# Kernel optimization log

Measured on AMD Instinct MI355X. Metric: run time of the kernel, lower is better.

The kernel has to match this reference:

```python
import jax, jax.numpy as jnp
import numpy as np

N, D, E, T, R, KMEM, DE = 50000, 128, 800000, 400000, 1, 32, 16
EPS = 1e-5
BETA_MAX = 5.0
GRAD_CLIP = 1.0
STATE_CLIP = 10.0
STEP = 0.1
DAMP = 0.9999  # update_damping=1.0 clamped to 1-1e-4 as in __init__


def segment_logsumexp(s, idx, n):
    # numerically-stable per-segment logsumexp; empty segments contribute 0
    m = jax.ops.segment_max(s, idx, num_segments=n)
    ms = jnp.where(jnp.isfinite(m), m, 0.0)
    z = jax.ops.segment_sum(jnp.exp(s - ms[idx]), idx, num_segments=n)
    return jnp.where(z > 0, jnp.log(jnp.maximum(z, 1e-30)) + ms, 0.0)


def setup_inputs() -> dict:
    key = jax.random.key(0)
    ks = jax.random.split(key, 24)
    inv1 = jnp.log(jnp.expm1(jnp.float32(1.0)))  # _inv_softplus(1.0)
    xav = 0.5 * np.sqrt(2.0 / (2 * D))  # xavier_uniform gain=0.5 ~ std
    inp = {
        'X': jax.random.normal(ks[0], (N, D), jnp.float32),
        'edge_attr': jax.random.normal(ks[1], (E, DE), jnp.float32),
        'ln_gamma': jnp.ones((D,), jnp.float32),
        'ln_beta': jnp.zeros((D,), jnp.float32),
        'W_Q2': jax.random.normal(ks[2], (D, D), jnp.float32) * xav,
        'W_K2': jax.random.normal(ks[3], (D, D), jnp.float32) * xav,
        'W_Q3': jax.random.normal(ks[4], (D, R * D), jnp.float32) * xav,
        'W_K3': jax.random.normal(ks[5], (D, R * D), jnp.float32) * xav,
        'T_tau': jax.random.normal(ks[6], (2, R, D), jnp.float32) * 0.02,
        'W_Qm': jax.random.normal(ks[7], (D, D), jnp.float32) * xav,
        'W_Km': jax.random.normal(ks[8], (D, D), jnp.float32) * xav,
        'B_mem': jax.random.normal(ks[9], (KMEM, D), jnp.float32) / np.sqrt(D),
        'We1': jax.random.normal(ks[10], (DE, D), jnp.float32) / np.sqrt(DE),
        'be1': jnp.zeros((D,), jnp.float32),
        'We2': jax.random.normal(ks[11], (D, 1), jnp.float32) / np.sqrt(D),
        'be2': jnp.zeros((1,), jnp.float32),
        'lambda_2': inv1, 'lambda_3': inv1, 'lambda_m': inv1,
        'beta_2': inv1, 'beta_3': inv1, 'beta_m': inv1,
        'c_2': jax.random.randint(ks[12], (E,), 0, N),
        'u_2': jax.random.randint(ks[13], (E,), 0, N),
        'c_3': jax.random.randint(ks[14], (T,), 0, N),
        'u_3': jax.random.randint(ks[15], (T,), 0, N),
        'v_3': jax.random.randint(ks[16], (T,), 0, N),
        't_tau': jax.random.randint(ks[17], (T,), 0, 2),
    }
    return inp


def reference(X, edge_attr, ln_gamma, ln_beta, W_Q2, W_K2, W_Q3, W_K3, T_tau,
              W_Qm, W_Km, B_mem, We1, be1, We2, be2,
              lambda_2, lambda_3, lambda_m, beta_2, beta_3, beta_m,
              c_2, u_2, c_3, u_3, v_3, t_tau):
    sqrt_d = jnp.sqrt(jnp.float32(D))

    def energy(Xv):
        mu = jnp.mean(Xv, axis=-1, keepdims=True)
        var = jnp.var(Xv, axis=-1, keepdims=True)
        G = (Xv - mu) * jax.lax.rsqrt(var + EPS) * ln_gamma + ln_beta
        # pairwise (order-2) energy over edge list
        b2 = jnp.minimum(jax.nn.softplus(beta_2), BETA_MAX)
        Q2, K2 = G @ W_Q2, G @ W_K2
        a2 = (jax.nn.gelu(edge_attr @ We1 + be1) @ We2 + be2)[:, 0]  # edge_mlp bias
        s2 = b2 * (jnp.sum(Q2[c_2] * K2[u_2], axis=-1) / sqrt_d) + a2  # [E]
        E2 = -(jax.nn.softplus(lambda_2) / b2) * jnp.sum(segment_logsumexp(s2, c_2, N))
        # triplet (order-3) energy with per-type tensor T_tau
        b3 = jnp.minimum(jax.nn.softplus(beta_3), BETA_MAX)
        Q3 = (G @ W_Q3).reshape(-1, R, D)
        K3 = (G @ W_K3).reshape(-1, R, D)
        s3 = b3 * jnp.einsum('erd,erd,erd,erd->e', Q3[c_3], K3[u_3], K3[v_3],
                             T_tau[t_tau]) / jnp.float32(D)  # [T]
        E3 = -(jax.nn.softplus(lambda_3) / b3) * jnp.sum(segment_logsumexp(s3, c_3, N))
        # memory-bank energy
        bm = jnp.minimum(jax.nn.softplus(beta_m), BETA_MAX)
        sm = bm * ((G @ W_Qm) @ (B_mem @ W_Km).T) / sqrt_d  # [N,K]
        Em = -(jax.nn.softplus(lambda_m) / bm) * jnp.sum(jax.nn.logsumexp(sm, axis=1))
        return E2 + E3 + Em

    Eval, gX = jax.value_and_grad(energy)(X)
    gn = jnp.maximum(jnp.linalg.norm(gX, axis=-1, keepdims=True), 1e-6)
    gX = gX * jnp.minimum(GRAD_CLIP / gn, 1.0)
    X_next = X - STEP * DAMP * gX
    sn = jnp.maximum(jnp.linalg.norm(X_next, axis=-1, keepdims=True), 1e-6)
    X_next = X_next * jnp.minimum(STATE_CLIP / sn, 1.0)
    return (X_next, Eval)
```

## Files before the change

### kernel.cpp

```cpp
#include <hip/hip_runtime.h>

#define NN 50000
#define DD 128
#define EE 800000
#define TT 400000
#define KM 32
#define UU 320
#define ROWB 12500
#define MB 782
#define EDGE_BLKS 3125
#define SCAN_TILE 2048
#define SCAN_NB ((NN + SCAN_TILE - 1) / SCAN_TILE)

static constexpr float INV_SQRT_D = 0.08838834764831845f;
static constexpr float INV_D = 1.f / 128.f;

typedef __attribute__((ext_vector_type(8))) short bf16x8;
typedef __attribute__((ext_vector_type(4))) float f32x4;
typedef unsigned short ushort_t;

__device__ __forceinline__ float softplus_f(float x) {
  return (x > 20.f) ? x : log1pf(__expf(x));
}

__device__ __forceinline__ float gelu_fast(float x) {
  float p = fmaf(0.044715f * x * x, x, x);
  float e = __expf(-1.5957691216057308f * p);
  return x * __builtin_amdgcn_rcpf(1.f + e);
}

__device__ __forceinline__ float wredsum(float v) {
#pragma unroll
  for (int m = 32; m; m >>= 1) v += __shfl_xor(v, m, 64);
// ... 8 lines not shown

__device__ __forceinline__ float blo(unsigned w) { return __uint_as_float(w << 16); }
__device__ __forceinline__ float bhi(unsigned w) { return __uint_as_float(w & 0xffff0000u); }
__device__ __forceinline__ unsigned pack_bf16(float a, float b) {
  unsigned ua = __float_as_uint(a); ua += 0x7fff + ((ua >> 16) & 1);
  unsigned ub = __float_as_uint(b); ub += 0x7fff + ((ub >> 16) & 1);
  return (ua >> 16) | (ub & 0xffff0000u);
}
__device__ __forceinline__ ushort_t bf16_1(float x) {
  unsigned u = __float_as_uint(x); u += 0x7fff + ((u >> 16) & 1);
  return (ushort_t)(u >> 16);
}
__device__ __forceinline__ void unp8(uint4 w, float* f) {
  f[0] = blo(w.x); f[1] = bhi(w.x); f[2] = blo(w.y); f[3] = bhi(w.y);
  f[4] = blo(w.z); f[5] = bhi(w.z); f[6] = blo(w.w); f[7] = bhi(w.w);
}
__device__ __forceinline__ uint4 pk8(const float* f) {
  uint4 r;
  r.x = pack_bf16(f[0], f[1]); r.y = pack_bf16(f[2], f[3]);
  r.z = pack_bf16(f[4], f[5]); r.w = pack_bf16(f[6], f[7]);
  return r;
}

__global__ void params_k(const float* l2, const float* l3, const float* lm,
                         const float* b2, const float* b3, const float* bm,
                         float* __restrict__ P) {
  if (threadIdx.x != 0) return;
  float B2 = fminf(softplus_f(b2[0]), 5.f);
  float B3 = fminf(softplus_f(b3[0]), 5.f);
  float Bm = fminf(softplus_f(bm[0]), 5.f);
  float S2 = softplus_f(l2[0]);
  float S3 = softplus_f(l3[0]);
  float Sm = softplus_f(lm[0]);
  P[0] = B2; P[1] = B3; P[2] = Bm;
  P[3] = -S2 * INV_SQRT_D; P[4] = -S3 * INV_D; P[5] = -Sm * INV_SQRT_D;
  P[6] = -S2 / B2; P[7] = -S3 / B3; P[8] = -Sm / Bm;
}

__global__ __launch_bounds__(256) void ln_fwd(const float* __restrict__ X,
                                              const float* __restrict__ gamma,
                                              const float* __restrict__ beta,
                                              unsigned* __restrict__ Gb,
                                              float* __restrict__ meanv,
                                              float* __restrict__ rstdv) {
  int row = blockIdx.x * 4 + (threadIdx.x >> 6);
  if (row >= NN) return;
  int l = threadIdx.x & 63;
  float2 x2 = *(const float2*)(X + row * DD + 2 * l);
  float mu = wredsum(x2.x + x2.y) * (1.f / DD);
  float d0 = x2.x - mu, d1 = x2.y - mu;
  float var = wredsum(d0 * d0 + d1 * d1) * (1.f / DD);
  float rstd = rsqrtf(var + 1e-5f);
  float2 g2 = *(const float2*)(gamma + 2 * l);
  float2 b2 = *(const float2*)(beta + 2 * l);
  float o0 = d0 * rstd * g2.x + b2.x;
  float o1 = d1 * rstd * g2.y + b2.y;
  Gb[(size_t)row * 64 + l] = pack_bf16(o0, o1);
  if (l == 0) { meanv[row] = mu; rstdv[row] = rstd; }
}

__global__ __launch_bounds__(256) void w_conv(const float* W0, const float* W1, const float* W2,
                                              const float* W3, const float* W4,
                                              ushort_t* __restrict__ Wt,
                                              ushort_t* __restrict__ Wc) {
  int idx = blockIdx.x * 256 + threadIdx.x;
  if (idx >= 640 * 128) return;
  const float* Ws[5] = {W0, W1, W2, W3, W4};
  int n = idx >> 7, k = idx & 127;
  Wt[idx] = bf16_1(Ws[n >> 7][(size_t)k * 128 + (n & 127)]);
  int k2 = idx >> 7, n2 = idx & 127;
  Wc[(size_t)n2 * 640 + k2] = bf16_1(Ws[k2 >> 7][(size_t)n2 * 128 + (k2 & 127)]);
}

__device__ void mfma_fwd_body(int bxr, int by, const ushort_t* __restrict__ Gb,
                              const ushort_t* __restrict__ Wt,
                              ushort_t* __restrict__ QK, int M) {
  __shared__ ushort_t sB[64][136];
  int tid = threadIdx.x;
  int nb = by * 64;
  for (int idx = tid; idx < 64 * 16; idx += 256) {
    int r = idx >> 4, c8 = idx & 15;
    *(bf16x8*)&sB[r][c8 * 8] = *(const bf16x8*)(Wt + (size_t)(nb + r) * 128 + c8 * 8);
  }
  __syncthreads();
  int w = tid >> 6, l = tid & 63, quad = l >> 4, j = l & 15;
  int row0 = bxr * 64 + w * 16;
  int arow = row0 + j; if (arow >= M) arow = M - 1;
  const bf16x8* ap = (const bf16x8*)(Gb + (size_t)arow * 128);
  f32x4 acc[4];
#pragma unroll
  for (int nt = 0; nt < 4; nt++) acc[nt] = (f32x4){0.f, 0.f, 0.f, 0.f};
#pragma unroll
  for (int kc = 0; kc < 4; kc++) {
    bf16x8 a = ap[kc * 4 + quad];
// ... 60 lines not shown
    float s0 = 0.f, s1 = 0.f, s2 = 0.f, s3 = 0.f;
#pragma unroll
    for (int nt = 0; nt < 8; nt++) {
      float bias = bb[nt];
      f32x4 cin = (f32x4){bias, bias, bias, bias};
      f32x4 acc = __builtin_amdgcn_mfma_f32_16x16x32_bf16(af.v, bf[nt].v, cin, 0, 0, 0);
      float w2v = ww[nt];
      s0 = fmaf(gelu_fast(acc[0]), w2v, s0);
      s1 = fmaf(gelu_fast(acc[1]), w2v, s1);
      s2 = fmaf(gelu_fast(acc[2]), w2v, s2);
      s3 = fmaf(gelu_fast(acc[3]), w2v, s3);
    }
    s0 = redsum16(s0); s1 = redsum16(s1); s2 = redsum16(s2); s3 = redsum16(s3);
    if (m == 0) {
      int eb = e0 + q * 4;
      a2[eb + 0] = s0 + be2v;
      a2[eb + 1] = s1 + be2v;
      a2[eb + 2] = s2 + be2v;
      a2[eb + 3] = s3 + be2v;
    }
  }
}

__global__ __launch_bounds__(256) void fwd_k(const ushort_t* __restrict__ Gb,
                                             const ushort_t* __restrict__ Wt,
                                             ushort_t* __restrict__ QK,
                                             const float* __restrict__ EA,
                                             const float* __restrict__ We1,
                                             const float* __restrict__ be1,
                                             const float* __restrict__ We2,
                                             const float* __restrict__ be2,
                                             float* __restrict__ a2) {
  int bx = blockIdx.x;
  if (bx < MB * 10) {
    mfma_fwd_body(bx / 10, bx % 10, Gb, Wt, QK, NN);
  } else {
    edge_mlp_body(bx - MB * 10, EA, We1, be1, We2, be2, a2);
  }
}

__global__ __launch_bounds__(256) void mfma_bwd(const ushort_t* __restrict__ dAll,
                                                const ushort_t* __restrict__ Wc,
                                                unsigned* __restrict__ dG, int M) {
  __shared__ ushort_t sB[64][40];
  int tid = threadIdx.x;
  int nb = blockIdx.y * 64;
  int w = tid >> 6, l = tid & 63, quad = l >> 4, j = l & 15;
  int row0 = blockIdx.x * 64 + w * 16;
  int arow = row0 + j; if (arow >= M) arow = M - 1;
  const ushort_t* arp = dAll + (size_t)arow * 640;
  f32x4 acc[4];
#pragma unroll
  for (int nt = 0; nt < 4; nt++) acc[nt] = (f32x4){0.f, 0.f, 0.f, 0.f};
  int sr = tid >> 2, sc = tid & 3;
  for (int kc = 0; kc < 20; kc++) {
    __syncthreads();
    *(bf16x8*)&sB[sr][sc * 8] = *(const bf16x8*)(Wc + (size_t)(nb + sr) * 640 + kc * 32 + sc * 8);
    __syncthreads();
    bf16x8 a = *(const bf16x8*)(arp + kc * 32 + quad * 8);
#pragma unroll
    for (int nt = 0; nt < 4; nt++) {
      bf16x8 b = *(const bf16x8*)&sB[nt * 16 + j][quad * 8];
      acc[nt] = __builtin_amdgcn_mfma_f32_16x16x32_bf16(a, b, acc[nt], 0, 0, 0);
    }
  }
#pragma unroll
  for (int nt = 0; nt < 4; nt++)
#pragma unroll
    for (int r = 0; r < 4; r++) {
      int row = row0 + quad * 4 + r;
      if (row < M) ((ushort_t*)dG)[(size_t)row * 128 + nb + nt * 16 + j] = bf16_1(acc[nt][r]);
    }
}

__global__ __launch_bounds__(256, 1) void gemm_km(const float* __restrict__ A,
                                                  const float* __restrict__ W,
                                                  float* __restrict__ C, int M) {
  __shared__ float As[32][132];
  __shared__ float Wst[128][136];
  const int tid = threadIdx.x;
  for (int idx = tid; idx < 128 * 128; idx += 256) {
    int k = idx >> 7, jj = idx & 127;
    Wst[k][jj] = W[k * 128 + jj];
  }
  for (int idx = tid; idx < 32 * 128; idx += 256) {
    int r = idx >> 7, d = idx & 127;
    As[r][d] = A[r * 128 + d];
  }
  __syncthreads();
  int r = tid >> 3, c0 = (tid & 7) * 16;
  float acc[16];
#pragma unroll
  for (int q = 0; q < 16; q++) acc[q] = 0.f;
  for (int k = 0; k < 128; k++) {
    float av = As[r][k];
#pragma unroll
    for (int q = 0; q < 16; q++) acc[q] = fmaf(av, Wst[k][c0 + q], acc[q]);
  }
#pragma unroll
  for (int q = 0; q < 16; q++) C[r * 128 + c0 + q] = acc[q];
}

__global__ __launch_bounds__(256) void hist2(const int* __restrict__ a,
                                             const int* __restrict__ b,
                                             int* __restrict__ ca,
                                             int* __restrict__ cb,
                                             int* __restrict__ pos_a,
                                             int* __restrict__ pos_b, int n) {
  int base = blockIdx.x * 2048 + threadIdx.x;
  if (base + 1792 < n) {
    int av[8], bv[8], pa[8], pb[8];
#pragma unroll
    for (int k = 0; k < 8; k++) { int e = base + k * 256; av[k] = a[e]; bv[k] = b[e]; }
#pragma unroll
    for (int k = 0; k < 8; k++) pa[k] = atomicAdd(&ca[av[k]], 1);
#pragma unroll
    for (int k = 0; k < 8; k++) pb[k] = atomicAdd(&cb[bv[k]], 1);
#pragma unroll
    for (int k = 0; k < 8; k++) pos_a[base + k * 256] = pa[k];
#pragma unroll
    for (int k = 0; k < 8; k++) pos_b[base + k * 256] = pb[k];
  } else {
#pragma unroll
    for (int k = 0; k < 8; k++) {
      int e = base + k * 256;
      if (e < n) {
        pos_a[e] = atomicAdd(&ca[a[e]], 1);
        pos_b[e] = atomicAdd(&cb[b[e]], 1);
      }
    }
  }
}

__global__ __launch_bounds__(256) void hist_t3(const int* __restrict__ c,
                                               const int* __restrict__ u,
                                               const int* __restrict__ v,
                                               int* __restrict__ cc,
                                               int* __restrict__ cuv,
                                               int* __restrict__ pos_c,
                                               int* __restrict__ pos_u,
                                               int* __restrict__ pos_v, int n) {
  int base = blockIdx.x * 2048 + threadIdx.x;
  if (base + 1792 < n) {
    int cv[8], uv[8], vv[8], pc[8], pu[8], pv[8];
#pragma unroll
    for (int k = 0; k < 8; k++) { int t = base + k * 256; cv[k] = c[t]; uv[k] = u[t]; vv[k] = v[t]; }
#pragma unroll
    for (int k = 0; k < 8; k++) pc[k] = atomicAdd(&cc[cv[k]], 1);
#pragma unroll
    for (int k = 0; k < 8; k++) pu[k] = atomicAdd(&cuv[uv[k]], 1);
#pragma unroll
    for (int k = 0; k < 8; k++) pv[k] = atomicAdd(&cuv[vv[k]], 1);
#pragma unroll
    for (int k = 0; k < 8; k++) pos_c[base + k * 256] = pc[k];
#pragma unroll
    for (int k = 0; k < 8; k++) pos_u[base + k * 256] = pu[k];
#pragma unroll
    for (int k = 0; k < 8; k++) pos_v[base + k * 256] = pv[k];
  } else {
#pragma unroll
    for (int k = 0; k < 8; k++) {
      int t = base + k * 256;
      if (t < n) {
        pos_c[t] = atomicAdd(&cc[c[t]], 1);
        pos_u[t] = atomicAdd(&cuv[u[t]], 1);
        pos_v[t] = atomicAdd(&cuv[v[t]], 1);
      }
    }
  }
}

__global__ __launch_bounds__(256) void scan_p1(const int* __restrict__ cnt,
                                               int* __restrict__ part) {
  int arr = blockIdx.y, b = blockIdx.x;
  const int* c = cnt + (size_t)arr * NN;
  int gi = b * SCAN_TILE + threadIdx.x * 8;
  int s = 0;
#pragma unroll
  for (int t = 0; t < 8; t++) s += (gi + t < NN) ? c[gi + t] : 0;
#pragma unroll
  for (int m = 32; m; m >>= 1) s += __shfl_xor(s, m, 64);
  __shared__ int wt[4];
  int lane = threadIdx.x & 63, wid = threadIdx.x >> 6;
  if (lane == 0) wt[wid] = s;
  __syncthreads();
  if (threadIdx.x == 0) part[arr * SCAN_NB + b] = wt[0] + wt[1] + wt[2] + wt[3];
}

__global__ __launch_bounds__(256) void scan_p2(int* __restrict__ part) {
  int w = threadIdx.x >> 6, l = threadIdx.x & 63;
  int v = (l < SCAN_NB) ? part[w * SCAN_NB + l] : 0;
  int x = v;
#pragma unroll
  for (int d = 1; d < 64; d <<= 1) {
// ... 18 lines not shown
#pragma unroll
  for (int t = 0; t < 8; t++) tsum += vals[t];
  int lane = tid & 63, wid = tid >> 6;
  int x = tsum;
#pragma unroll
  for (int d = 1; d < 64; d <<= 1) {
    int y = __shfl_up(x, d, 64);
    if (lane >= d) x += y;
  }
  __shared__ int wt[4];
  if (lane == 63) wt[wid] = x;
  __syncthreads();
  int wadd = 0;
  for (int w = 0; w < wid; w++) wadd += wt[w];
  int running = part[arr * SCAN_NB + b] + wadd + x - tsum;
#pragma unroll
  for (int t = 0; t < 8; t++) {
    if (gi + t < NN) rp[gi + t] = running;
    running += vals[t];
  }
  if (b == SCAN_NB - 1 && tid == 255) rp[NN] = running;
}

__global__ __launch_bounds__(256) void scat2(const int* __restrict__ c2,
                                             const int* __restrict__ u2,
                                             const float* __restrict__ a2,
                                             const int* __restrict__ posc,
                                             const int* __restrict__ posu,
                                             const int* __restrict__ rpc,
                                             const int* __restrict__ rpu,
                                             uint2* __restrict__ payc,
                                             uint2* __restrict__ payu, int n) {
  int base = blockIdx.x * 2048 + threadIdx.x;
  if (base + 1792 < n) {
    int c[8], u[8]; float a[8]; int pc[8], pu[8];
#pragma unroll
    for (int k = 0; k < 8; k++) {
      int e = base + k * 256;
      c[k] = c2[e]; u[k] = u2[e]; a[k] = a2[e]; pc[k] = posc[e]; pu[k] = posu[e];
    }
    int p[8], q[8];
#pragma unroll
    for (int k = 0; k < 8; k++) { p[k] = rpc[c[k]] + pc[k]; q[k] = rpu[u[k]] + pu[k]; }
#pragma unroll
    for (int k = 0; k < 8; k++) {
      uint2 t; t.x = (unsigned)u[k]; t.y = __float_as_uint(a[k]);
      payc[p[k]] = t;
    }
#pragma unroll
    for (int k = 0; k < 8; k++) {
      uint2 t; t.x = (unsigned)p[k]; t.y = (unsigned)c[k];
      payu[q[k]] = t;
    }
  } else {
#pragma unroll
    for (int k = 0; k < 8; k++) {
      int e = base + k * 256;
      if (e < n) {
        int cc = c2[e], uu = u2[e];
        int pp = rpc[cc] + posc[e];
        int qq = rpu[uu] + posu[e];
        uint2 t; t.x = (unsigned)uu; t.y = __float_as_uint(a2[e]);
        payc[pp] = t;
        uint2 t2; t2.x = (unsigned)pp; t2.y = (unsigned)cc;
        payu[qq] = t2;
      }
    }
  }
}

__global__ __launch_bounds__(256) void scat_t3(const int* __restrict__ c3,
                                               const int* __restrict__ u3,
                                               const int* __restrict__ v3,
                                               const int* __restrict__ ttau,
                                               const int* __restrict__ posc,
                                               const int* __restrict__ posu,
                                               const int* __restrict__ posv,
                                               const int* __restrict__ rpc,
                                               const int* __restrict__ rpuv,
                                               uint2* __restrict__ payc,
                                               uint2* __restrict__ payuv, int n) {
  int base = blockIdx.x * 2048 + threadIdx.x;
  if (base + 1792 < n) {
    int c[8], u[8], v[8], ta[8], p[8], q1[8], q2[8];
#pragma unroll
    for (int k = 0; k < 8; k++) {
      int t = base + k * 256;
      c[k] = c3[t]; u[k] = u3[t]; v[k] = v3[t]; ta[k] = ttau[t] & 1;
    }
#pragma unroll
    for (int k = 0; k < 8; k++) {
      int t = base + k * 256;
      p[k] = rpc[c[k]] + posc[t];
      q1[k] = rpuv[u[k]] + posu[t];
      q2[k] = rpuv[v[k]] + posv[t];
    }
#pragma unroll
    for (int k = 0; k < 8; k++) {
      uint2 a; a.x = ((unsigned)u[k] << 16) | (unsigned)v[k]; a.y = (unsigned)ta[k];
      payc[p[k]] = a;
    }
#pragma unroll
    for (int k = 0; k < 8; k++) {
      unsigned sp = ((unsigned)p[k] << 1) | (unsigned)ta[k];
      uint2 b1; b1.x = ((unsigned)v[k] << 16) | (unsigned)c[k]; b1.y = sp;
      payuv[q1[k]] = b1;
      uint2 b2; b2.x = ((unsigned)u[k] << 16) | (unsigned)c[k]; b2.y = sp;
      payuv[q2[k]] = b2;
    }
  } else {
#pragma unroll
    for (int k = 0; k < 8; k++) {
      int t = base + k * 256;
      if (t < n) {
        int c = c3[t], u = u3[t], v = v3[t], ta = ttau[t] & 1;
        int p = rpc[c] + posc[t];
        int q1 = rpuv[u] + posu[t];
        int q2 = rpuv[v] + posv[t];
        unsigned sp = ((unsigned)p << 1) | (unsigned)ta;
        uint2 a; a.x = ((unsigned)u << 16) | (unsigned)v; a.y = (unsigned)ta;
        payc[p] = a;
        uint2 b1; b1.x = ((unsigned)v << 16) | (unsigned)c; b1.y = sp;
        payuv[q1] = b1;
        uint2 b2; b2.x = ((unsigned)u << 16) | (unsigned)c; b2.y = sp;
        payuv[q2] = b2;
      }
    }
  }
}

__device__ void e2_body(int bx, const unsigned* __restrict__ QK,
                        const float* __restrict__ P,
                        const uint2* __restrict__ pay,
                        const int* __restrict__ rp,
                        float* __restrict__ s2c,
                        float* __restrict__ L2,
                        unsigned* __restrict__ dAll) {
  int row = bx * 4 + (threadIdx.x >> 6);
  int l = threadIdx.x & 63, g = l >> 4, j = l & 15;
  float b2s = P[0] * INV_SQRT_D, cw2 = P[3];
  float q[8];
  unp8(*(const uint4*)(QK + (size_t)row * UU + j * 4), q);
  int s = rp[row], e = rp[row + 1];
  float m = -3.0e38f, z = 0.f;
  float acc[8] = {0.f, 0.f, 0.f, 0.f, 0.f, 0.f, 0.f, 0.f};
  int i0 = s + g;
  uint4 kA1 = {0,0,0,0}, kA2 = {0,0,0,0}, kB1 = {0,0,0,0}, kB2 = {0,0,0,0};
  float aA1 = 0.f, aA2 = 0.f, aB1 = 0.f, aB2 = 0.f;
  if (i0 < e)      { uint2 w = pay[i0];      aA1 = __uint_as_float(w.y); kA1 = *(const uint4*)(QK + (size_t)w.x * UU + 64 + j * 4); }
  if (i0 + 4 < e)  { uint2 w = pay[i0 + 4];  aA2 = __uint_as_float(w.y); kA2 = *(const uint4*)(QK + (size_t)w.x * UU + 64 + j * 4); }
// ... 204 lines not shown
    v += __shfl_xor(v, 16, 64);
    v += __shfl_xor(v, 32, 64);
    acc[t] = v;
  }
  if (g == 0) *(uint4*)(dAll + (size_t)row * UU + 256 + j * 4) = pk8(acc);
}

__global__ __launch_bounds__(256) void phase2_k(const unsigned* __restrict__ QK,
                                                const float* __restrict__ Tt,
                                                const float* __restrict__ Km,
                                                const float* __restrict__ P,
                                                const uint2* __restrict__ payc2,
                                                const int* __restrict__ rp_c2,
                                                const uint2* __restrict__ payc3,
                                                const int* __restrict__ rp_c3,
                                                float* __restrict__ s2c,
                                                float* __restrict__ L2,
                                                float* __restrict__ s3c,
                                                float* __restrict__ L3,
                                                float* __restrict__ Lm,
                                                unsigned* __restrict__ dAll) {
  __shared__ float smem[32 * 144];
  int bx = blockIdx.x;
  int tid = threadIdx.x;
  if (bx < ROWB) {
    e2_body(bx, QK, P, payc2, rp_c2, s2c, L2, dAll);
  } else if (bx < 2 * ROWB) {
    {
      int ta = tid >> 7, d = tid & 127;
      smem[ta * 144 + (d >> 3) * 9 + (d & 7)] = Tt[tid];
    }
    __syncthreads();
    t3_body(bx - ROWB, QK, P, payc3, rp_c3, s3c, L3, dAll, smem);
  } else {
    for (int i = tid; i < KM * DD; i += 256) {
      int k = i >> 7, d = i & 127;
      smem[k * 144 + (d >> 3) * 9 + (d & 7)] = Km[i];
    }
    __syncthreads();
    em_body(bx - 2 * ROWB, QK, P, dAll, Lm, smem);
  }
}

__device__ void dk2_body(int bx, const unsigned* __restrict__ QK,
                         const float* __restrict__ s2c,
                         const float* __restrict__ L2,
                         const float* __restrict__ P,
                         const uint2* __restrict__ pay,
                         const int* __restrict__ rp,
                         unsigned* __restrict__ dAll) {
  int row = bx * 4 + (threadIdx.x >> 6);
  int l = threadIdx.x & 63, g = l >> 4, j = l & 15;
  float cw2 = P[3];
  int s = rp[row], e = rp[row + 1];
  float acc[8] = {0.f, 0.f, 0.f, 0.f, 0.f, 0.f, 0.f, 0.f};
  int i0 = s + g;
  uint4 qA1 = {0,0,0,0}, qA2 = {0,0,0,0}, qB1 = {0,0,0,0}, qB2 = {0,0,0,0};
  float scA1 = 0.f, lcA1 = 0.f, scA2 = 0.f, lcA2 = 0.f;
  float scB1 = 0.f, lcB1 = 0.f, scB2 = 0.f, lcB2 = 0.f;
  if (i0 < e)      { uint2 w = pay[i0];      scA1 = s2c[w.x]; lcA1 = L2[w.y]; qA1 = *(const uint4*)(QK + (size_t)w.y * UU + 0 + j * 4); }
  if (i0 + 4 < e)  { uint2 w = pay[i0 + 4];  scA2 = s2c[w.x]; lcA2 = L2[w.y]; qA2 = *(const uint4*)(QK + (size_t)w.y * UU + 0 + j * 4); }
  if (i0 + 8 < e)  { uint2 w = pay[i0 + 8];  scB1 = s2c[w.x]; lcB1 = L2[w.y]; qB1 = *(const uint4*)(QK + (size_t)w.y * UU + 0 + j * 4); }
  if (i0 + 12 < e) { uint2 w = pay[i0 + 12]; scB2 = s2c[w.x]; lcB2 = L2[w.y]; qB2 = *(const uint4*)(QK + (size_t)w.y * UU + 0 + j * 4); }
// ... 79 lines not shown
  for (int t = 0; t < 8; t++) {
    float v = acc[t];
    v += __shfl_xor(v, 16, 64);
    v += __shfl_xor(v, 32, 64);
    acc[t] = v;
  }
  if (g == 0) *(uint4*)(dAll + (size_t)row * UU + 192 + j * 4) = pk8(acc);
}

__global__ __launch_bounds__(256) void phase3_k(const unsigned* __restrict__ QK,
                                                const float* __restrict__ Tt,
                                                const float* __restrict__ P,
                                                const float* __restrict__ s2c,
                                                const float* __restrict__ L2,
                                                const uint2* __restrict__ payu2,
                                                const int* __restrict__ rp_u2,
                                                const float* __restrict__ s3c,
                                                const float* __restrict__ L3,
                                                const uint2* __restrict__ payuv,
                                                const int* __restrict__ rp_uv,
                                                unsigned* __restrict__ dAll) {
  __shared__ float smem[2 * 144];
  int bx = blockIdx.x;
  int tid = threadIdx.x;
  if (bx < ROWB) {
    dk2_body(bx, QK, s2c, L2, P, payu2, rp_u2, dAll);
  } else {
    {
      int ta = tid >> 7, d = tid & 127;
      smem[ta * 144 + (d >> 3) * 9 + (d & 7)] = Tt[tid];
    }
    __syncthreads();
    dk3_body(bx - ROWB, QK, s3c, L3, P, payuv, rp_uv, dAll, smem);
  }
}

__global__ __launch_bounds__(256) void ln_bwd(const float* __restrict__ X,
                                              const unsigned* __restrict__ dG,
                                              const float* __restrict__ gamma,
                                              const float* __restrict__ meanv,
                                              const float* __restrict__ rstdv,
                                              float* __restrict__ out) {
  int row = blockIdx.x * 4 + (threadIdx.x >> 6);
  if (row >= NN) return;
  int l = threadIdx.x & 63;
  float mu = meanv[row], rstd = rstdv[row];
  float2 x2 = *(const float2*)(X + row * DD + 2 * l);
  unsigned gw = dG[(size_t)row * 64 + l];
  float2 ga = *(const float2*)(gamma + 2 * l);
  float xh0 = (x2.x - mu) * rstd, xh1 = (x2.y - mu) * rstd;
  float dh0 = blo(gw) * ga.x, dh1 = bhi(gw) * ga.y;
  float sa = wredsum(dh0 + dh1) * (1.f / DD);
  float sb = wredsum(dh0 * xh0 + dh1 * xh1) * (1.f / DD);
  float dx0 = rstd * (dh0 - sa - xh0 * sb);
  float dx1 = rstd * (dh1 - sa - xh1 * sb);
  float gn = fmaxf(sqrtf(wredsum(dx0 * dx0 + dx1 * dx1)), 1e-6f);
  float sc = fminf(1.f / gn, 1.f);
  dx0 *= sc; dx1 *= sc;
  float xn0 = x2.x - 0.1f * 0.9999f * dx0;
  float xn1 = x2.y - 0.1f * 0.9999f * dx1;
  float sn = fmaxf(sqrtf(wredsum(xn0 * xn0 + xn1 * xn1)), 1e-6f);
  float sc2 = fminf(10.f / sn, 1.f);
  float2 o; o.x = xn0 * sc2; o.y = xn1 * sc2;
  *(float2*)(out + row * DD + 2 * l) = o;
}

__global__ __launch_bounds__(256) void eval_write(const float* __restrict__ L2,
                                                  const float* __restrict__ L3,
                                                  const float* __restrict__ Lm,
                                                  const float* __restrict__ P,
                                                  float* __restrict__ out) {
  int i = blockIdx.x * 256 + threadIdx.x;
  float a2 = 0.f, a3 = 0.f, am = 0.f;
  if (i < NN) { a2 = L2[i]; a3 = L3[i]; am = Lm[i]; }
  a2 = wredsum(a2); a3 = wredsum(a3); am = wredsum(am);
  __shared__ float r2[4], r3[4], rm[4];
  int wv = threadIdx.x >> 6, l = threadIdx.x & 63;
  if (l == 0) { r2[wv] = a2; r3[wv] = a3; rm[wv] = am; }
  __syncthreads();
  if (threadIdx.x == 0) {
    float S2 = r2[0] + r2[1] + r2[2] + r2[3];
    float S3 = r3[0] + r3[1] + r3[2] + r3[3];
    float Sm = rm[0] + rm[1] + rm[2] + rm[3];
    atomicAdd(out, P[6] * S2 + P[7] * S3 + P[8] * Sm);
  }
}

extern "C" void kernel_launch(void* const* d_in, const int* in_sizes, int n_in,
                              void* d_out, int out_size, void* d_ws, size_t ws_size,
                              hipStream_t stream) {
  (void)in_sizes; (void)n_in; (void)out_size;
  const float* X = (const float*)d_in[0];
  const float* EA = (const float*)d_in[1];
  const float* ln_g = (const float*)d_in[2];
  const float* ln_b = (const float*)d_in[3];
  const float* W_Q2 = (const float*)d_in[4];
  const float* W_K2 = (const float*)d_in[5];
  const float* W_Q3 = (const float*)d_in[6];
  const float* W_K3 = (const float*)d_in[7];
  const float* T_tau = (const float*)d_in[8];
  const float* W_Qm = (const float*)d_in[9];
  const float* W_Km = (const float*)d_in[10];
  const float* B_mem = (const float*)d_in[11];
  const float* We1 = (const float*)d_in[12];
  const float* be1 = (const float*)d_in[13];
  const float* We2 = (const float*)d_in[14];
  const float* be2 = (const float*)d_in[15];
  const float* l2s = (const float*)d_in[16];
// ... 27 lines not shown
  float* meanv = alloc(NN);
  float* rstdv = alloc(NN);
  float* L2 = alloc(NN);
  float* L3 = alloc(NN);
  float* Lm = alloc(NN);
  float* Pparams = alloc(16);
  int* cnt = (int*)alloc(4 * (size_t)NN);
  int* rowptr = (int*)alloc(4 * (size_t)(NN + 1));
  int* spart = (int*)alloc(4 * SCAN_NB);
  int* pos_c2 = (int*)alloc(EE);
  int* pos_u2 = (int*)alloc(EE);
  int* pos_c3 = (int*)alloc(TT);
  int* pos_u3 = (int*)alloc(TT);
  int* pos_v3 = (int*)alloc(TT);
  uint2* payc2 = (uint2*)alloc(2 * (size_t)EE);
  uint2* payu2 = (uint2*)alloc(2 * (size_t)EE);
  uint2* payc3 = (uint2*)alloc(2 * (size_t)TT);
  uint2* payuv = (uint2*)alloc(4 * (size_t)TT);
  if (off * sizeof(float) > ws_size) return;

  int* cnt_c2 = cnt, *cnt_u2 = cnt + NN, *cnt_c3 = cnt + 2 * NN, *cnt_uv = cnt + 3 * NN;
  int* rp_c2 = rowptr, *rp_u2 = rowptr + (NN + 1), *rp_c3 = rowptr + 2 * (NN + 1), *rp_uv = rowptr + 3 * (NN + 1);

  hipMemsetAsync(cnt, 0, 4ull * NN * sizeof(int), stream);
  hipMemsetAsync(out + ND, 0, sizeof(float), stream);

  params_k<<<1, 64, 0, stream>>>(l2s, l3s, lms, b2s, b3s, bms, Pparams);

  int rowB = ROWB;

  ln_fwd<<<rowB, 256, 0, stream>>>(X, ln_g, ln_b, Gb, meanv, rstdv);
  w_conv<<<320, 256, 0, stream>>>(W_Q2, W_K2, W_Q3, W_K3, W_Qm, Wt5, Wcat);
  gemm_km<<<1, 256, 0, stream>>>(B_mem, W_Km, Km, KM);
  fwd_k<<<MB * 10 + EDGE_BLKS, 256, 0, stream>>>((const ushort_t*)Gb, Wt5, (ushort_t*)QKall,
                                                 EA, We1, be1, We2, be2, a2);

  hist2<<<(EE + 2047) / 2048, 256, 0, stream>>>(c2, u2, cnt_c2, cnt_u2, pos_c2, pos_u2, EE);
  hist_t3<<<(TT + 2047) / 2048, 256, 0, stream>>>(c3, u3, v3, cnt_c3, cnt_uv,
                                                  pos_c3, pos_u3, pos_v3, TT);
  scan_p1<<<dim3(SCAN_NB, 4), 256, 0, stream>>>(cnt, spart);
  scan_p2<<<1, 256, 0, stream>>>(spart);
  scan_p3<<<dim3(SCAN_NB, 4), 256, 0, stream>>>(cnt, spart, rowptr);
  scat2<<<(EE + 2047) / 2048, 256, 0, stream>>>(c2, u2, a2, pos_c2, pos_u2,
                                                rp_c2, rp_u2, payc2, payu2, EE);
  scat_t3<<<(TT + 2047) / 2048, 256, 0, stream>>>(c3, u3, v3, ttau,
                                                  pos_c3, pos_u3, pos_v3,
                                                  rp_c3, rp_uv, payc3, payuv, TT);

  phase2_k<<<3 * ROWB, 256, 0, stream>>>(QKall, T_tau, Km, Pparams,
                                         payc2, rp_c2, payc3, rp_c3,
                                         s2c, L2, s3c, L3, Lm, dAll);
  phase3_k<<<2 * ROWB, 256, 0, stream>>>(QKall, T_tau, Pparams,
                                         s2c, L2, payu2, rp_u2,
                                         s3c, L3, payuv, rp_uv, dAll);

  mfma_bwd<<<dim3(MB, 2), 256, 0, stream>>>((const ushort_t*)dAll, Wcat, dG, NN);

  ln_bwd<<<rowB, 256, 0, stream>>>(X, dG, ln_g, meanv, rstdv, out);
  eval_write<<<(NN + 255) / 256, 256, 0, stream>>>(L2, L3, Lm, Pparams, out + ND);
}
```

Measured before the change: 766.9 us.

## Merge small kernels into fused multi-role launches and interleave phase block roles

Measured after the change: 765.2 us. No clear change (-0.2%).

```diff
diff --git a/kernel.cpp b/kernel.cpp
--- a/kernel.cpp
+++ b/kernel.cpp
@@ -9,6 +9,10 @@
 #define ROWB 12500
 #define MB 782
 #define EDGE_BLKS 3125
+#define HB2 391
+#define HBT 196
+#define WCB 320
+#define ZCB 196
 #define SCAN_TILE 2048
 #define SCAN_NB ((NN + SCAN_TILE - 1) / SCAN_TILE)
 
@@ -63,28 +67,13 @@
   return r;
 }
 
-__global__ void params_k(const float* l2, const float* l3, const float* lm,
-                         const float* b2, const float* b3, const float* bm,
-                         float* __restrict__ P) {
-  if (threadIdx.x != 0) return;
-  float B2 = fminf(softplus_f(b2[0]), 5.f);
-  float B3 = fminf(softplus_f(b3[0]), 5.f);
-  float Bm = fminf(softplus_f(bm[0]), 5.f);
-  float S2 = softplus_f(l2[0]);
-  float S3 = softplus_f(l3[0]);
-  float Sm = softplus_f(lm[0]);
-  P[0] = B2; P[1] = B3; P[2] = Bm;
-  P[3] = -S2 * INV_SQRT_D; P[4] = -S3 * INV_D; P[5] = -Sm * INV_SQRT_D;
-  P[6] = -S2 / B2; P[7] = -S3 / B3; P[8] = -Sm / Bm;
-}
-
-__global__ __launch_bounds__(256) void ln_fwd(const float* __restrict__ X,
-                                              const float* __restrict__ gamma,
-                                              const float* __restrict__ beta,
-                                              unsigned* __restrict__ Gb,
-                                              float* __restrict__ meanv,
-                                              float* __restrict__ rstdv) {
-  int row = blockIdx.x * 4 + (threadIdx.x >> 6);
+__device__ void ln_fwd_body(int bx, const float* __restrict__ X,
+                            const float* __restrict__ gamma,
+                            const float* __restrict__ beta,
+                            unsigned* __restrict__ Gb,
+                            float* __restrict__ meanv,
+                            float* __restrict__ rstdv) {
+  int row = bx * 4 + (threadIdx.x >> 6);
   if (row >= NN) return;
   int l = threadIdx.x & 63;
   float2 x2 = *(const float2*)(X + row * DD + 2 * l);
@@ -100,17 +89,87 @@
   if (l == 0) { meanv[row] = mu; rstdv[row] = rstd; }
 }
 
-__global__ __launch_bounds__(256) void w_conv(const float* W0, const float* W1, const float* W2,
-                                              const float* W3, const float* W4,
-                                              ushort_t* __restrict__ Wt,
-                                              ushort_t* __restrict__ Wc) {
-  int idx = blockIdx.x * 256 + threadIdx.x;
-  if (idx >= 640 * 128) return;
+__device__ void w_conv_body(int b, const float* W0, const float* W1, const float* W2,
+                            const float* W3, const float* W4,
+                            ushort_t* __restrict__ Wt,
+                            ushort_t* __restrict__ Wc) {
+  int idx = b * 256 + threadIdx.x;
   const float* Ws[5] = {W0, W1, W2, W3, W4};
   int n = idx >> 7, k = idx & 127;
   Wt[idx] = bf16_1(Ws[n >> 7][(size_t)k * 128 + (n & 127)]);
   int k2 = idx >> 7, n2 = idx & 127;
   Wc[(size_t)n2 * 640 + k2] = bf16_1(Ws[k2 >> 7][(size_t)n2 * 128 + (k2 & 127)]);
+}
+
+__device__ void gemm_km_lean(const float* __restrict__ A,
+                             const float* __restrict__ W,
+                             float* __restrict__ C) {
+  __shared__ float As[32][129];
+  int tid = threadIdx.x;
+  for (int idx = tid; idx < 32 * 128; idx += 256) As[idx >> 7][idx & 127] = A[idx];
+  __syncthreads();
+  int r = tid >> 3, c0 = (tid & 7) * 16;
+  float acc[16];
+#pragma unroll
+  for (int q = 0; q < 16; q++) acc[q] = 0.f;
+  for (int k = 0; k < 128; k++) {
+    float av = As[r][k];
+#pragma unroll
+    for (int q = 0; q < 16; q++) acc[q] = fmaf(av, W[k * 128 + c0 + q], acc[q]);
+  }
+#pragma unroll
+  for (int q = 0; q < 16; q++) C[r * 128 + c0 + q] = acc[q];
+}
+
+__global__ __launch_bounds__(256) void prep_k(const float* __restrict__ X,
+                                              const float* __restrict__ ln_g,
+                                              const float* __restrict__ ln_b,
+                                              unsigned* __restrict__ Gb,
+                                              float* __restrict__ meanv,
+                                              float* __restrict__ rstdv,
+                                              const float* W0, const float* W1,
+                                              const float* W2, const float* W3,
+                                              const float* W4,
+                                              ushort_t* __restrict__ Wt,
+                                              ushort_t* __restrict__ Wc,
+                                              const float* __restrict__ Bm,
+                                              const float* __restrict__ Wkm,
+                                              float* __restrict__ Km,
+                                              const float* l2, const float* l3,
+                                              const float* lm, const float* b2,
+                                              const float* b3, const float* bm,
+                                              float* __restrict__ P,
+                                              float* __restrict__ eout,
+                                              int* __restrict__ cnt) {
+  int bx = blockIdx.x, tid = threadIdx.x;
+  if (bx < ROWB) {
+    ln_fwd_body(bx, X, ln_g, ln_b, Gb, meanv, rstdv);
+  } else if (bx < ROWB + WCB) {
+    w_conv_body(bx - ROWB, W0, W1, W2, W3, W4, Wt, Wc);
+  } else if (bx == ROWB + WCB) {
+    gemm_km_lean(Bm, Wkm, Km);
+  } else if (bx == ROWB + WCB + 1) {
+    if (tid == 0) {
+      float B2 = fminf(softplus_f(b2[0]), 5.f);
+      float B3 = fminf(softplus_f(b3[0]), 5.f);
+      float Bm_ = fminf(softplus_f(bm[0]), 5.f);
+      float S2 = softplus_f(l2[0]);
+      float S3 = softplus_f(l3[0]);
+      float Sm = softplus_f(lm[0]);
+      P[0] = B2; P[1] = B3; P[2] = Bm_;
+      P[3] = -S2 * INV_SQRT_D; P[4] = -S3 * INV_D; P[5] = -Sm * INV_SQRT_D;
+      P[6] = -S2 / B2; P[7] = -S3 / B3; P[8] = -Sm / Bm_;
+    }
+    if (tid == 1) eout[0] = 0.f;
+  } else {
+    int i = (bx - (ROWB + WCB + 2)) * 1024 + tid * 4;
+    if (i + 3 < 4 * NN) {
+      *(int4*)&cnt[i] = (int4){0, 0, 0, 0};
+    } else {
+#pragma unroll
+      for (int t = 0; t < 4; t++) if (i + t < 4 * NN) cnt[i + t] = 0;
+    }
+  }
 }
 
 __device__ void mfma_fwd_body(int bxr, int by, const ushort_t* __restrict__ Gb,
@@ -217,6 +276,71 @@
   }
 }
 
+__device__ void hist2_body(int bx, const int* __restrict__ a,
+                           const int* __restrict__ b,
+                           int* __restrict__ ca, int* __restrict__ cb,
+                           int* __restrict__ pos_a, int* __restrict__ pos_b, int n) {
+  int base = bx * 2048 + threadIdx.x;
+  if (base + 1792 < n) {
+    int av[8], bv[8], pa[8], pb[8];
+#pragma unroll
+    for (int k = 0; k < 8; k++) { int e = base + k * 256; av[k] = a[e]; bv[k] = b[e]; }
+#pragma unroll
+    for (int k = 0; k < 8; k++) pa[k] = atomicAdd(&ca[av[k]], 1);
+#pragma unroll
+    for (int k = 0; k < 8; k++) pb[k] = atomicAdd(&cb[bv[k]], 1);
+#pragma unroll
+    for (int k = 0; k < 8; k++) pos_a[base + k * 256] = pa[k];
+#pragma unroll
+    for (int k = 0; k < 8; k++) pos_b[base + k * 256] = pb[k];
+  } else {
+#pragma unroll
+    for (int k = 0; k < 8; k++) {
+      int e = base + k * 256;
+      if (e < n) {
+        pos_a[e] = atomicAdd(&ca[a[e]], 1);
+        pos_b[e] = atomicAdd(&cb[b[e]], 1);
+      }
+    }
+  }
+}
+
+__device__ void hist_t3_body(int bx, const int* __restrict__ c,
+                             const int* __restrict__ u,
+                             const int* __restrict__ v,
+                             int* __restrict__ cc, int* __restrict__ cuv,
+                             int* __restrict__ pos_c, int* __restrict__ pos_u,
+                             int* __restrict__ pos_v, int n) {
+  int base = bx * 2048 + threadIdx.x;
+  if (base + 1792 < n) {
+    int cv[8], uv[8], vv[8], pc[8], pu[8], pv[8];
+#pragma unroll
+    for (int k = 0; k < 8; k++) { int t = base + k * 256; cv[k] = c[t]; uv[k] = u[t]; vv[k] = v[t]; }
+#pragma unroll
+    for (int k = 0; k < 8; k++) pc[k] = atomicAdd(&cc[cv[k]], 1);
+#pragma unroll
+    for (int k = 0; k < 8; k++) pu[k] = atomicAdd(&cuv[uv[k]], 1);
+#pragma unroll
+    for (int k = 0; k < 8; k++) pv[k] = atomicAdd(&cuv[vv[k]], 1);
+#pragma unroll
+    for (int k = 0; k < 8; k++) pos_c[base + k * 256] = pc[k];
+#pragma unroll
+    for (int k = 0; k < 8; k++) pos_u[base + k * 256] = pu[k];
+#pragma unroll
+    for (int k = 0; k < 8; k++) pos_v[base + k * 256] = pv[k];
+  } else {
+#pragma unroll
+    for (int k = 0; k < 8; k++) {
+      int t = base + k * 256;
+      if (t < n) {
+        pos_c[t] = atomicAdd(&cc[c[t]], 1);
+        pos_u[t] = atomicAdd(&cuv[u[t]], 1);
+        pos_v[t] = atomicAdd(&cuv[v[t]], 1);
+      }
+    }
+  }
+}
+
 __global__ __launch_bounds__(256) void fwd_k(const ushort_t* __restrict__ Gb,
                                              const ushort_t* __restrict__ Wt,
                                              ushort_t* __restrict__ QK,
@@ -225,12 +349,31 @@
                                              const float* __restrict__ be1,
                                              const float* __restrict__ We2,
                                              const float* __restrict__ be2,
-                                             float* __restrict__ a2) {
+                                             float* __restrict__ a2,
+                                             const int* __restrict__ c2,
+                                             const int* __restrict__ u2,
+                                             const int* __restrict__ c3,
+                                             const int* __restrict__ u3,
+                                             const int* __restrict__ v3,
+                                             int* __restrict__ cnt_c2,
+                                             int* __restrict__ cnt_u2,
+                                             int* __restrict__ cnt_c3,
+                                             int* __restrict__ cnt_uv,
+                                             int* __restrict__ pos_c2,
+                                             int* __restrict__ pos_u2,
+                                             int* __restrict__ pos_c3,
+                                             int* __restrict__ pos_u3,
+                                             int* __restrict__ pos_v3) {
   int bx = blockIdx.x;
-  if (bx < MB * 10) {
-    mfma_fwd_body(bx / 10, bx % 10, Gb, Wt, QK, NN);
+  if (bx < HB2) {
+    hist2_body(bx, c2, u2, cnt_c2, cnt_u2, pos_c2, pos_u2, EE);
+  } else if (bx < HB2 + HBT) {
+    hist_t3_body(bx - HB2, c3, u3, v3, cnt_c3, cnt_uv, pos_c3, pos_u3, pos_v3, TT);
+  } else if (bx < HB2 + HBT + MB * 10) {
+    int b = bx - HB2 - HBT;
+    mfma_fwd_body(b / 10, b % 10, Gb, Wt, QK, NN);
   } else {
-    edge_mlp_body(bx - MB * 10, EA, We1, be1, We2, be2, a2);
+    edge_mlp_body(bx - HB2 - HBT - MB * 10, EA, We1, be1, We2, be2, a2);
   }
 }
 
@@ -268,103 +411,6 @@
     }
 }
 
-__global__ __launch_bounds__(256, 1) void gemm_km(const float* __restrict__ A,
-                                                  const float* __restrict__ W,
-                                                  float* __restrict__ C, int M) {
-  __shared__ float As[32][132];
-  __shared__ float Wst[128][136];
-  const int tid = threadIdx.x;
-  for (int idx = tid; idx < 128 * 128; idx += 256) {
-    int k = idx >> 7, jj = idx & 127;
-    Wst[k][jj] = W[k * 128 + jj];
-  }
-  for (int idx = tid; idx < 32 * 128; idx += 256) {
-    int r = idx >> 7, d = idx & 127;
-    As[r][d] = A[r * 128 + d];
-  }
-  __syncthreads();
-  int r = tid >> 3, c0 = (tid & 7) * 16;
-  float acc[16];
-#pragma unroll
-  for (int q = 0; q < 16; q++) acc[q] = 0.f;
-  for (int k = 0; k < 128; k++) {
-    float av = As[r][k];
-#pragma unroll
-    for (int q = 0; q < 16; q++) acc[q] = fmaf(av, Wst[k][c0 + q], acc[q]);
-  }
-#pragma unroll
-  for (int q = 0; q < 16; q++) C[r * 128 + c0 + q] = acc[q];
-}
-
-__global__ __launch_bounds__(256) void hist2(const int* __restrict__ a,
-                                             const int* __restrict__ b,
-                                             int* __restrict__ ca,
-                                             int* __restrict__ cb,
-                                             int* __restrict__ pos_a,
-                                             int* __restrict__ pos_b, int n) {
-  int base = blockIdx.x * 2048 + threadIdx.x;
-  if (base + 1792 < n) {
-    int av[8], bv[8], pa[8], pb[8];
-#pragma unroll
-    for (int k = 0; k < 8; k++) { int e = base + k * 256; av[k] = a[e]; bv[k] = b[e]; }
-#pragma unroll
-    for (int k = 0; k < 8; k++) pa[k] = atomicAdd(&ca[av[k]], 1);
-#pragma unroll
-    for (int k = 0; k < 8; k++) pb[k] = atomicAdd(&cb[bv[k]], 1);
-#pragma unroll
-    for (int k = 0; k < 8; k++) pos_a[base + k * 256] = pa[k];
-#pragma unroll
-    for (int k = 0; k < 8; k++) pos_b[base + k * 256] = pb[k];
-  } else {
-#pragma unroll
-    for (int k = 0; k < 8; k++) {
-      int e = base + k * 256;
-      if (e < n) {
-        pos_a[e] = atomicAdd(&ca[a[e]], 1);
-        pos_b[e] = atomicAdd(&cb[b[e]], 1);
-      }
-    }
-  }
-}
-
-__global__ __launch_bounds__(256) void hist_t3(const int* __restrict__ c,
-                                               const int* __restrict__ u,
-                                               const int* __restrict__ v,
-                                               int* __restrict__ cc,
-                                               int* __restrict__ cuv,
-                                               int* __restrict__ pos_c,
-                                               int* __restrict__ pos_u,
-                                               int* __restrict__ pos_v, int n) {
-  int base = blockIdx.x * 2048 + threadIdx.x;
-  if (base + 1792 < n) {
-    int cv[8], uv[8], vv[8], pc[8], pu[8], pv[8];
-#pragma unroll
-    for (int k = 0; k < 8; k++) { int t = base + k * 256; cv[k] = c[t]; uv[k] = u[t]; vv[k] = v[t]; }
-#pragma unroll
-    for (int k = 0; k < 8; k++) pc[k] = atomicAdd(&cc[cv[k]], 1);
-#pragma unroll
-    for (int k = 0; k < 8; k++) pu[k] = atomicAdd(&cuv[uv[k]], 1);
-#pragma unroll
-    for (int k = 0; k < 8; k++) pv[k] = atomicAdd(&cuv[vv[k]], 1);
-#pragma unroll
-    for (int k = 0; k < 8; k++) pos_c[base + k * 256] = pc[k];
-#pragma unroll
-    for (int k = 0; k < 8; k++) pos_u[base + k * 256] = pu[k];
-#pragma unroll
-    for (int k = 0; k < 8; k++) pos_v[base + k * 256] = pv[k];
-  } else {
-#pragma unroll
-    for (int k = 0; k < 8; k++) {
-      int t = base + k * 256;
-      if (t < n) {
-        pos_c[t] = atomicAdd(&cc[c[t]], 1);
-        pos_u[t] = atomicAdd(&cuv[u[t]], 1);
-        pos_v[t] = atomicAdd(&cuv[v[t]], 1);
-      }
-    }
-  }
-}
-
 __global__ __launch_bounds__(256) void scan_p1(const int* __restrict__ cnt,
                                                int* __restrict__ part) {
   int arr = blockIdx.y, b = blockIdx.x;
@@ -429,16 +475,16 @@
   if (b == SCAN_NB - 1 && tid == 255) rp[NN] = running;
 }
 
-__global__ __launch_bounds__(256) void scat2(const int* __restrict__ c2,
-                                             const int* __restrict__ u2,
-                                             const float* __restrict__ a2,
-                                             const int* __restrict__ posc,
-                                             const int* __restrict__ posu,
-                                             const int* __restrict__ rpc,
-                                             const int* __restrict__ rpu,
-                                             uint2* __restrict__ payc,
-                                             uint2* __restrict__ payu, int n) {
-  int base = blockIdx.x * 2048 + threadIdx.x;
+__device__ void scat2_body(int bx, const int* __restrict__ c2,
+                           const int* __restrict__ u2,
+                           const float* __restrict__ a2,
+                           const int* __restrict__ posc,
+                           const int* __restrict__ posu,
+                           const int* __restrict__ rpc,
+                           const int* __restrict__ rpu,
+                           uint2* __restrict__ payc,
+                           uint2* __restrict__ payu, int n) {
+  int base = bx * 2048 + threadIdx.x;
   if (base + 1792 < n) {
     int c[8], u[8]; float a[8]; int pc[8], pu[8];
 #pragma unroll
@@ -476,18 +522,18 @@
   }
 }
 
-__global__ __launch_bounds__(256) void scat_t3(const int* __restrict__ c3,
-                                               const int* __restrict__ u3,
-                                               const int* __restrict__ v3,
-                                               const int* __restrict__ ttau,
-                                               const int* __restrict__ posc,
-                                               const int* __restrict__ posu,
-                                               const int* __restrict__ posv,
-                                               const int* __restrict__ rpc,
-                                               const int* __restrict__ rpuv,
-                                               uint2* __restrict__ payc,
-                                               uint2* __restrict__ payuv, int n) {
-  int base = blockIdx.x * 2048 + threadIdx.x;
+__device__ void scat_t3_body(int bx, const int* __restrict__ c3,
+                             const int* __restrict__ u3,
+                             const int* __restrict__ v3,
+                             const int* __restrict__ ttau,
+                             const int* __restrict__ posc,
+                             const int* __restrict__ posu,
+                             const int* __restrict__ posv,
+                             const int* __restrict__ rpc,
+                             const int* __restrict__ rpuv,
+                             uint2* __restrict__ payc,
+                             uint2* __restrict__ payuv, int n) {
+  int base = bx * 2048 + threadIdx.x;
   if (base + 1792 < n) {
     int c[8], u[8], v[8], ta[8], p[8], q1[8], q2[8];
 #pragma unroll
@@ -533,6 +579,35 @@
         payuv[q2] = b2;
       }
     }
+  }
+}
+
+__global__ __launch_bounds__(256) void scat_k(const int* __restrict__ c2,
+                                              const int* __restrict__ u2,
+                                              const float* __restrict__ a2,
+                                              const int* __restrict__ pos_c2,
+                                              const int* __restrict__ pos_u2,
+                                              const int* __restrict__ rp_c2,
+                                              const int* __restrict__ rp_u2,
+                                              uint2* __restrict__ payc2,
+                                              uint2* __restrict__ payu2,
+                                              const int* __restrict__ c3,
+                                              const int* __restrict__ u3,
+                                              const int* __restrict__ v3,
+                                              const int* __restrict__ ttau,
+                                              const int* __restrict__ pos_c3,
+                                              const int* __restrict__ pos_u3,
+                                              const int* __restrict__ pos_v3,
+                                              const int* __restrict__ rp_c3,
+                                              const int* __restrict__ rp_uv,
+                                              uint2* __restrict__ payc3,
+                                              uint2* __restrict__ payuv) {
+  int bx = blockIdx.x;
+  if (bx < HB2) {
+    scat2_body(bx, c2, u2, a2, pos_c2, pos_u2, rp_c2, rp_u2, payc2, payu2, EE);
+  } else {
+    scat_t3_body(bx - HB2, c3, u3, v3, ttau, pos_c3, pos_u3, pos_v3,
+                 rp_c3, rp_uv, payc3, payuv, TT);
   }
 }
 
@@ -783,23 +858,24 @@
                                                 unsigned* __restrict__ dAll) {
   __shared__ float smem[32 * 144];
   int bx = blockIdx.x;
+  int body = bx % 3, b = bx / 3;
   int tid = threadIdx.x;
-  if (bx < ROWB) {
-    e2_body(bx, QK, P, payc2, rp_c2, s2c, L2, dAll);
-  } else if (bx < 2 * ROWB) {
+  if (body == 0) {
+    e2_body(b, QK, P, payc2, rp_c2, s2c, L2, dAll);
+  } else if (body == 1) {
     {
       int ta = tid >> 7, d = tid & 127;
       smem[ta * 144 + (d >> 3) * 9 + (d & 7)] = Tt[tid];
     }
     __syncthreads();
-    t3_body(bx - ROWB, QK, P, payc3, rp_c3, s3c, L3, dAll, smem);
+    t3_body(b, QK, P, payc3, rp_c3, s3c, L3, dAll, smem);
   } else {
     for (int i = tid; i < KM * DD; i += 256) {
       int k = i >> 7, d = i & 127;
       smem[k * 144 + (d >> 3) * 9 + (d & 7)] = Km[i];
     }
     __syncthreads();
-    em_body(bx - 2 * ROWB, QK, P, dAll, Lm, smem);
+    em_body(b, QK, P, dAll, Lm, smem);
   }
 }
 
@@ -925,26 +1001,27 @@
                                                 unsigned* __restrict__ dAll) {
   __shared__ float smem[2 * 144];
   int bx = blockIdx.x;
+  int body = bx & 1, b = bx >> 1;
   int tid = threadIdx.x;
-  if (bx < ROWB) {
-    dk2_body(bx, QK, s2c, L2, P, payu2, rp_u2, dAll);
+  if (body == 0) {
+    dk2_body(b, QK, s2c, L2, P, payu2, rp_u2, dAll);
   } else {
     {
       int ta = tid >> 7, d = tid & 127;
       smem[ta * 144 + (d >> 3) * 9 + (d & 7)] = Tt[tid];
     }
     __syncthreads();
-    dk3_body(bx - ROWB, QK, s3c, L3, P, payuv, rp_uv, dAll, smem);
-  }
-}
-
-__global__ __launch_bounds__(256) void ln_bwd(const float* __restrict__ X,
-                                              const unsigned* __restrict__ dG,
-                                              const float* __restrict__ gamma,
-                                              const float* __restrict__ meanv,
-                                              const float* __restrict__ rstdv,
-                                              float* __restrict__ out) {
-  int row = blockIdx.x * 4 + (threadIdx.x >> 6);
+    dk3_body(b, QK, s3c, L3, P, payuv, rp_uv, dAll, smem);
+  }
+}
+
+__device__ void ln_bwd_body(int bx, const float* __restrict__ X,
+                            const unsigned* __restrict__ dG,
+                            const float* __restrict__ gamma,
+                            const float* __restrict__ meanv,
+                            const float* __restrict__ rstdv,
+                            float* __restrict__ out) {
+  int row = bx * 4 + (threadIdx.x >> 6);
   if (row >= NN) return;
   int l = threadIdx.x & 63;
   float mu = meanv[row], rstd = rstdv[row];
@@ -968,12 +1045,12 @@
   *(float2*)(out + row * DD + 2 * l) = o;
 }
 
-__global__ __launch_bounds__(256) void eval_write(const float* __restrict__ L2,
-                                                  const float* __restrict__ L3,
-                                                  const float* __restrict__ Lm,
-                                                  const float* __restrict__ P,
-                                                  float* __restrict__ out) {
-  int i = blockIdx.x * 256 + threadIdx.x;
+__device__ void eval_write_body(int bx, const float* __restrict__ L2,
+                                const float* __restrict__ L3,
+                                const float* __restrict__ Lm,
+                                const float* __restrict__ P,
+                                float* __restrict__ out) {
+  int i = bx * 256 + threadIdx.x;
   float a2 = 0.f, a3 = 0.f, am = 0.f;
   if (i < NN) { a2 = L2[i]; a3 = L3[i]; am = Lm[i]; }
   a2 = wredsum(a2); a3 = wredsum(a3); am = wredsum(am);
@@ -987,6 +1064,22 @@
     float Sm = rm[0] + rm[1] + rm[2] + rm[3];
     atomicAdd(out, P[6] * S2 + P[7] * S3 + P[8] * Sm);
   }
+}
+
+__global__ __launch_bounds__(256) void fin_k(const float* __restrict__ X,
+                                             const unsigned* __restrict__ dG,
+                                             const float* __restrict__ gamma,
+                                             const float* __restrict__ meanv,
+                                             const float* __restrict__ rstdv,
+                                             float* __restrict__ out,
+                                             const float* __restrict__ L2,
+                                             const float* __restrict__ L3,
+                                             const float* __restrict__ Lm,
+                                             const float* __restrict__ P,
+                                             float* __restrict__ eout) {
+  int bx = blockIdx.x;
+  if (bx < ROWB) ln_bwd_body(bx, X, dG, gamma, meanv, rstdv, out);
+  else eval_write_body(bx - ROWB, L2, L3, Lm, P, eout);
 }
 
 extern "C" void kernel_launch(void* const* d_in, const int* in_sizes, int n_in,
@@ -1060,30 +1153,26 @@
   int* cnt_c2 = cnt, *cnt_u2 = cnt + NN, *cnt_c3 = cnt + 2 * NN, *cnt_uv = cnt + 3 * NN;
   int* rp_c2 = rowptr, *rp_u2 = rowptr + (NN + 1), *rp_c3 = rowptr + 2 * (NN + 1), *rp_uv = rowptr + 3 * (NN + 1);
 
-  hipMemsetAsync(cnt, 0, 4ull * NN * sizeof(int), stream);
-  hipMemsetAsync(out + ND, 0, sizeof(float), stream);
-
-  params_k<<<1, 64, 0, stream>>>(l2s, l3s, lms, b2s, b3s, bms, Pparams);
-
-  int rowB = ROWB;
-
-  ln_fwd<<<rowB, 256, 0, stream>>>(X, ln_g, ln_b, Gb, meanv, rstdv);
-  w_conv<<<320, 256, 0, stream>>>(W_Q2, W_K2, W_Q3, W_K3, W_Qm, Wt5, Wcat);
-  gemm_km<<<1, 256, 0, stream>>>(B_mem, W_Km, Km, KM);
-  fwd_k<<<MB * 10 + EDGE_BLKS, 256, 0, stream>>>((const ushort_t*)Gb, Wt5, (ushort_t*)QKall,
-                                                 EA, We1, be1, We2, be2, a2);
-
-  hist2<<<(EE + 2047) / 2048, 256, 0, stream>>>(c2, u2, cnt_c2, cnt_u2, pos_c2, pos_u2, EE);
-  hist_t3<<<(TT + 2047) / 2048, 256, 0, stream>>>(c3, u3, v3, cnt_c3, cnt_uv,
-                                                  pos_c3, pos_u3, pos_v3, TT);
+  prep_k<<<ROWB + WCB + 2 + ZCB, 256, 0, stream>>>(
+      X, ln_g, ln_b, Gb, meanv, rstdv,
+      W_Q2, W_K2, W_Q3, W_K3, W_Qm, Wt5, Wcat,
+      B_mem, W_Km, Km,
+      l2s, l3s, lms, b2s, b3s, bms, Pparams, out + ND, cnt);
+
+  fwd_k<<<HB2 + HBT + MB * 10 + EDGE_BLKS, 256, 0, stream>>>(
+      (const ushort_t*)Gb, Wt5, (ushort_t*)QKall,
+      EA, We1, be1, We2, be2, a2,
+      c2, u2, c3, u3, v3,
+      cnt_c2, cnt_u2, cnt_c3, cnt_uv,
+      pos_c2, pos_u2, pos_c3, pos_u3, pos_v3);
+
   scan_p1<<<dim3(SCAN_NB, 4), 256, 0, stream>>>(cnt, spart);
   scan_p2<<<1, 256, 0, stream>>>(spart);
   scan_p3<<<dim3(SCAN_NB, 4), 256, 0, stream>>>(cnt, spart, rowptr);
-  scat2<<<(EE + 2047) / 2048, 256, 0, stream>>>(c2, u2, a2, pos_c2, pos_u2,
-                                                rp_c2, rp_u2, payc2, payu2, EE);
-  scat_t3<<<(TT + 2047) / 2048, 256, 0, stream>>>(c3, u3, v3, ttau,
-                                                  pos_c3, pos_u3, pos_v3,
-                                                  rp_c3, rp_uv, payc3, payuv, TT);
+
+  scat_k<<<HB2 + HBT, 256, 0, stream>>>(
+      c2, u2, a2, pos_c2, pos_u2, rp_c2, rp_u2, payc2, payu2,
+      c3, u3, v3, ttau, pos_c3, pos_u3, pos_v3, rp_c3, rp_uv, payc3, payuv);
 
   phase2_k<<<3 * ROWB, 256, 0, stream>>>(QKall, T_tau, Km, Pparams,
                                          payc2, rp_c2, payc3, rp_c3,
@@ -1094,6 +1183,6 @@
 
   mfma_bwd<<<dim3(MB, 2), 256, 0, stream>>>((const ushort_t*)dAll, Wcat, dG, NN);
 
-  ln_bwd<<<rowB, 256, 0, stream>>>(X, dG, ln_g, meanv, rstdv, out);
-  eval_write<<<(NN + 255) / 256, 256, 0, stream>>>(L2, L3, Lm, Pparams, out + ND);
-}
+  fin_k<<<ROWB + 196, 256, 0, stream>>>(X, dG, ln_g, meanv, rstdv, out,
+                                        L2, L3, Lm, Pparams, out + ND);
+}
```
